# Performance work log

Measured on AMD Instinct MI355X. Metric: run time of the kernel, lower is better.

Reference implementation:

```python
import jax, jax.numpy as jnp
import numpy as np

D_MODEL = 1024
NUM_HEADS = 16
HEAD_DIM = D_MODEL // NUM_HEADS
ROPE_BASE = 10000.0


def setup_inputs() -> dict:
    key = jax.random.key(0)
    ks = jax.random.split(key, 9)
    B, S = 2, 2048
    x = jax.random.normal(ks[0], (B, S, D_MODEL), dtype=jnp.float32)
    s = 1.0 / np.sqrt(D_MODEL)
    Wq = jax.random.normal(ks[1], (D_MODEL, D_MODEL), dtype=jnp.float32) * s
    bq = jnp.zeros((D_MODEL,), dtype=jnp.float32)
    Wk = jax.random.normal(ks[2], (D_MODEL, D_MODEL), dtype=jnp.float32) * s
    bk = jnp.zeros((D_MODEL,), dtype=jnp.float32)
    Wv = jax.random.normal(ks[3], (D_MODEL, D_MODEL), dtype=jnp.float32) * s
    bv = jnp.zeros((D_MODEL,), dtype=jnp.float32)
    Wo = jax.random.normal(ks[4], (D_MODEL, D_MODEL), dtype=jnp.float32) * s
    bo = jnp.zeros((D_MODEL,), dtype=jnp.float32)
    return {"x": x, "Wq": Wq, "bq": bq, "Wk": Wk, "bk": bk,
            "Wv": Wv, "bv": bv, "Wo": Wo, "bo": bo}


def _apply_rope(x):
    # x: [B, H, S, Dh]; interleaved complex-pair RoPE (torch.view_as_complex style)
    B, H, S, Dh = x.shape
    inv_freq = 1.0 / (ROPE_BASE ** (jnp.arange(0, Dh, 2, dtype=jnp.float32) / Dh))
    pos = jnp.arange(S, dtype=jnp.float32)
    freqs = pos[:, None] * inv_freq[None, :]            # [S, Dh/2]
    cos, sin = jnp.cos(freqs), jnp.sin(freqs)           # each [S, Dh/2]
    x2 = x.reshape(B, H, S, Dh // 2, 2)
    xr, xi = x2[..., 0], x2[..., 1]
    out_r = xr * cos - xi * sin
    out_i = xr * sin + xi * cos
    return jnp.stack([out_r, out_i], axis=-1).reshape(B, H, S, Dh)


def reference(x, Wq, bq, Wk, bk, Wv, bv, Wo, bo):
    B, S, _ = x.shape
    H, Dh = NUM_HEADS, HEAD_DIM
    def proj(W, b):
        y = jnp.einsum('bsd,ed->bse', x, W) + b          # torch Linear: x @ W.T + b
        return y.reshape(B, S, H, Dh).transpose(0, 2, 1, 3)  # [B,H,S,Dh]
    Q = _apply_rope(proj(Wq, bq))
    K = _apply_rope(proj(Wk, bk))
    V = proj(Wv, bv)
    scale = 1.0 / jnp.sqrt(jnp.float32(Dh))
    scores = jnp.einsum('bhqd,bhkd->bhqk', Q, K) * scale
    causal = jnp.tril(jnp.ones((S, S), dtype=bool))
    scores = jnp.where(causal, scores, jnp.float32(-jnp.inf))
    attn = jax.nn.softmax(scores, axis=-1)
    out = jnp.einsum('bhqk,bhkd->bhqd', attn, V)         # [B,H,S,Dh]
    out = out.transpose(0, 2, 1, 3).reshape(B, S, H * Dh)
    return jnp.einsum('bsd,ed->bse', out, Wo) + bo
```

## Files before the change

### kernel.cpp

```cpp
#include <hip/hip_runtime.h>
#include <stdint.h>

#define S_LEN 2048
#define BATCH 2
#define DM 1024
#define NH 16
#define DH 64
#define MROWS 4096

typedef unsigned short u16;
typedef unsigned int u32;
typedef __attribute__((ext_vector_type(8))) short bf16x8;
typedef __attribute__((ext_vector_type(4))) float f32x4;
typedef __attribute__((ext_vector_type(2))) unsigned u32x2;

union pack8 { u32 w[4]; bf16x8 v8; };

__device__ inline u16 f2bf(float f) {
  union { float f; unsigned u; } v; v.f = f;
  unsigned u = v.u;
  unsigned r = u + 0x7fffu + ((u >> 16) & 1u);
  return (u16)(r >> 16);
}

__device__ inline u32 pkbf(float lo, float hi) {
  u32 r;
  asm("v_cvt_pk_bf16_f32 %0, %1, %2" : "=v"(r) : "v"(lo), "v"(hi));
  return r;
}

__device__ inline float bf2f(short s) {
  union { u32 u; float f; } c; c.u = ((u32)(u16)s) << 16;
  return c.f;
}

__device__ __forceinline__ void gload_lds16(const u16* g, u16* l) {
  __builtin_amdgcn_global_load_lds(
      (const __attribute__((address_space(1))) u32*)g,
      (__attribute__((address_space(3))) u32*)l, 16, 0, 0);
}

__global__ void convert_k(const float* __restrict__ x, const float* __restrict__ wq,
                          const float* __restrict__ wk, const float* __restrict__ wv,
                          const float* __restrict__ wo, u16* __restrict__ xb,
                          u16* __restrict__ wb) {
  int i = blockIdx.x * blockDim.x + threadIdx.x;
  const int total = (MROWS * DM + 4 * DM * DM) / 4;
  if (i >= total) return;
  int e = i * 4;
  const float* src;
  u16* dst;
  if (e < MROWS * DM) {
    src = x + e; dst = xb + e;
  } else {
    int j = e - MROWS * DM;
    int w = j >> 20;
    int o = j & ((1 << 20) - 1);
    src = (w == 0) ? wq + o : (w == 1) ? wk + o : (w == 2) ? wv + o : wo + o;
    dst = wb + j;
  }
  float4 v = *(const float4*)src;
  uint2 r;
  r.x = (unsigned)f2bf(v.x) | ((unsigned)f2bf(v.y) << 16);
  r.y = (unsigned)f2bf(v.z) | ((unsigned)f2bf(v.w) << 16);
  *(uint2*)dst = r;
}

__global__ void rope_k(float2* __restrict__ tab, float* __restrict__ kmax) {
  int i = blockIdx.x * blockDim.x + threadIdx.x;
  if (i < 32) kmax[i] = 0.f;
  if (i >= S_LEN * 32) return;
  int s = i >> 5, p = i & 31;
  float inv = expf(-(float)p * 0.28782313662425575f);
  float a = (float)s * inv;
  tab[i] = make_float2(cosf(a), sinf(a));
}

__global__ void knorm_k(const u16* __restrict__ K, float* __restrict__ kmax) {
  const int row = blockIdx.x * 256 + threadIdx.x;
  const int bh = row >> 11;
  const u16* p = K + (size_t)row * DH;
  float ss = 0.f;
#pragma unroll
  for (int i = 0; i < 8; i++) {
    bf16x8 v = *(const bf16x8*)(p + i * 8);
#pragma unroll
    for (int j = 0; j < 8; j++) { float f = bf2f(v[j]); ss += f * f; }
  }
  float kn = sqrtf(ss);
#pragma unroll
  for (int d = 1; d < 64; d <<= 1) kn = fmaxf(kn, __shfl_xor(kn, d));
  if ((threadIdx.x & 63) == 0)
    atomicMax((unsigned*)(kmax + bh), __float_as_uint(kn));
}

__launch_bounds__(256)
__global__ void gemm_k(const u16* __restrict__ A,
                       const u16* __restrict__ w0, const u16* __restrict__ w1,
                       const u16* __restrict__ w2,
                       const float* __restrict__ b0, const float* __restrict__ b1,
                       const float* __restrict__ b2,
                       const float2* __restrict__ rope,
                       void* __restrict__ o0, void* __restrict__ o1, void* __restrict__ o2,
                       int mode0) {
  const int mode = mode0 + (int)(blockIdx.x >> 8);
  const int tile = blockIdx.x & 255;
  const int mt = tile >> 3, nt = tile & 7;
  const int mbase = mt * 128, nbase = nt * 128;
  const u16* W = (mode == 1) ? w1 : (mode == 2) ? w2 : w0;
  const float* bias = (mode == 1) ? b1 : (mode == 2) ? b2 : b0;
  void* outp = (mode == 1) ? o1 : (mode == 2) ? o2 : o0;

  __shared__ u16 As[128 * 32];
  __shared__ u16 Bs[128 * 32];

  const int t = threadIdx.x;
  const int lane = t & 63, wvi = t >> 6;
  const int lr = lane & 15, lg = lane >> 4;
  const int wm = (wvi >> 1) * 64, wn = (wvi & 1) * 64;

  f32x4 acc[4][4] = {};
  const int srow = t >> 2;
  const int scol = (t & 3) * 8;

  for (int kk = 0; kk < DM; kk += 32) {
    gload_lds16(A + (size_t)(mbase + srow) * DM + kk + scol, &As[wvi * 512]);
    gload_lds16(A + (size_t)(mbase + 64 + srow) * DM + kk + scol, &As[2048 + wvi * 512]);
    gload_lds16(W + (size_t)(nbase + srow) * DM + kk + scol, &Bs[wvi * 512]);
    gload_lds16(W + (size_t)(nbase + 64 + srow) * DM + kk + scol, &Bs[2048 + wvi * 512]);
    __syncthreads();

    bf16x8 af[4], bfr[4];
#pragma unroll
    for (int mi = 0; mi < 4; mi++)
      af[mi] = *(const bf16x8*)&As[(wm + mi * 16 + lr) * 32 + lg * 8];
#pragma unroll
    for (int ni = 0; ni < 4; ni++)
      bfr[ni] = *(const bf16x8*)&Bs[(wn + ni * 16 + lr) * 32 + lg * 8];
#pragma unroll
    for (int mi = 0; mi < 4; mi++)
#pragma unroll
      for (int ni = 0; ni < 4; ni++)
        acc[mi][ni] = __builtin_amdgcn_mfma_f32_16x16x32_bf16(af[mi], bfr[ni], acc[mi][ni], 0, 0, 0);
    __syncthreads();
  }

#pragma unroll
  for (int ni = 0; ni < 4; ni++) {
    const int col = nbase + wn + ni * 16 + lr;
    const float bv = bias[col];
#pragma unroll
    for (int mi = 0; mi < 4; mi++) {
      const int row0 = mbase + wm + mi * 16 + lg * 4;
      f32x4 v = acc[mi][ni];
#pragma unroll
      for (int r = 0; r < 4; r++) {
        float val = v[r] + bv;
        const int row = row0 + r;
        if (mode <= 1) {
          float nb = __shfl_xor(val, 1);
          const int d = col & 63, p = d >> 1, s = row & (S_LEN - 1);
          float2 cs = rope[s * 32 + p];
          float ov = (d & 1) ? (nb * cs.y + val * cs.x) : (val * cs.x - nb * cs.y);
          if (mode == 0) ov *= 0.18033688011112042f;
          const int b = row >> 11, h = col >> 6;
          ((u16*)outp)[((size_t)(b * NH + h) * S_LEN + s) * DH + d] = f2bf(ov);
        } else if (mode == 2) {
          const int b = row >> 11, h = col >> 6, d = col & 63, s = row & (S_LEN - 1);
          const int j = s & 31;
          const int pos = (s & ~31) + (((j & 15) >> 2) << 3) + ((j >> 4) << 2) + (j & 3);
          ((u16*)outp)[((size_t)(b * NH + h) * DH + d) * S_LEN + pos] = f2bf(val);
        } else {
          ((float*)outp)[(size_t)row * DM + col] = val;
        }
      }
    }
  }
}

__device__ __forceinline__ void sm_pv(const float a[8], float m, float& l,
                                      bf16x8 v0, bf16x8 v1, bf16x8 v2, bf16x8 v3,
                                      f32x4* o) {
  float p[8];
#pragma unroll
  for (int r = 0; r < 8; r++) p[r] = __builtin_amdgcn_exp2f(a[r] - m);
  l += ((p[0] + p[1]) + (p[2] + p[3])) + ((p[4] + p[5]) + (p[6] + p[7]));
  pack8 pu;
  pu.w[0] = pkbf(p[0], p[1]);
  pu.w[1] = pkbf(p[2], p[3]);
  pu.w[2] = pkbf(p[4], p[5]);
  pu.w[3] = pkbf(p[6], p[7]);
  o[0] = __builtin_amdgcn_mfma_f32_16x16x32_bf16(v0, pu.v8, o[0], 0, 0, 0);
  o[1] = __builtin_amdgcn_mfma_f32_16x16x32_bf16(v1, pu.v8, o[1], 0, 0, 0);
  o[2] = __builtin_amdgcn_mfma_f32_16x16x32_bf16(v2, pu.v8, o[2], 0, 0, 0);
  o[3] = __builtin_amdgcn_mfma_f32_16x16x32_bf16(v3, pu.v8, o[3], 0, 0, 0);
}

__launch_bounds__(64)
__global__ void attn_k(const u16* __restrict__ Q, const u16* __restrict__ K,
                       const u16* __restrict__ Vt, u16* __restrict__ Oo,
                       const float* __restrict__ kmax,
                       u16* __restrict__ po, float* __restrict__ pl) {
  int bh, tile, s0, s1, pidx = 0, split;
  if (blockIdx.x < 1024) {
    bh = blockIdx.x & 31; tile = (int)(blockIdx.x >> 5);
    s0 = 0; s1 = tile + 1; split = 0;
  } else {
    const int idx = (int)blockIdx.x - 1024;
    bh = idx & 31; tile = 32 + ((idx >> 5) & 31);
    const int half = idx >> 10;
    const int nst = tile + 1, h = nst >> 1;
    s0 = half ? h : 0; s1 = half ? nst : h;
    pidx = idx; split = 1;
  }
  const int qbase = tile * 32;
  const int lane = threadIdx.x;
  const int lr = lane & 15, lg = lane >> 4;

  __shared__ u16 Ks[2][2048];
  __shared__ u16 Vs[2][2048];

  const u16* Kg = K + (size_t)bh * S_LEN * DH;
  const u16* Vg = Vt + (size_t)bh * DH * S_LEN;

  const int krow = lane >> 3;
  const int ksoff = ((((lane & 7) << 4) ^ ((lane >> 3) << 4)) >> 1);
  const int vrow = lane >> 2;
  const int vsoff = ((((lane & 3) << 4) ^ (((lane >> 3) & 3) << 4)) >> 1);

  const size_t qoff = ((size_t)bh * S_LEN + qbase + lr) * DH + lg * 8;
  const bf16x8 qA0 = *(const bf16x8*)(Q + qoff);
  const bf16x8 qA1 = *(const bf16x8*)(Q + qoff + 32);
  const bf16x8 qB0 = *(const bf16x8*)(Q + qoff + 16 * DH);
  const bf16x8 qB1 = *(const bf16x8*)(Q + qoff + 16 * DH + 32);

  float ssA = 0.f, ssB = 0.f;
#pragma unroll
  for (int j = 0; j < 8; j++) {
    float a0 = bf2f(qA0[j]), a1 = bf2f(qA1[j]);
    float b0 = bf2f(qB0[j]), b1 = bf2f(qB1[j]);
    ssA += a0 * a0 + a1 * a1;
    ssB += b0 * b0 + b1 * b1;
  }
  ssA += __shfl_xor(ssA, 16); ssA += __shfl_xor(ssA, 32);
  ssB += __shfl_xor(ssB, 16); ssB += __shfl_xor(ssB, 32);
  const float kmx = kmax[bh];
  const float mA = sqrtf(ssA) * kmx;
  const float mB = sqrtf(ssB) * kmx;

  f32x4 oA[4] = {}, oB[4] = {};
  float lA = 0.f, lB = 0.f;
  const f32x4 zero = {};

  const int kmsk = (lr & 7) << 4;
  const int k00 = lr * 64 + (((lg << 4)) ^ kmsk) / 2;
  const int k01 = lr * 64 + ((64 + (lg << 4)) ^ kmsk) / 2;
  const int k10 = (16 + lr) * 64 + (((lg << 4)) ^ kmsk) / 2;
  const int k11 = (16 + lr) * 64 + ((64 + (lg << 4)) ^ kmsk) / 2;
  const int vmsk = ((lr >> 1) & 3) << 4;
  const int vo = ((lg << 4) ^ vmsk) / 2;

#define STAGE(s32, bb)                                                          \
  {                                                                             \
    const u16* kgs = Kg + (size_t)(s32) * DH;                                   \
    const u16* vgs = Vg + (s32);                                                \
    _Pragma("unroll")                                                           \
    for (int i = 0; i < 4; i++)                                                 \
      gload_lds16(kgs + (size_t)(i * 8 + krow) * DH + ksoff, &Ks[bb][i * 512]); \
    _Pragma("unroll")                                                           \
    for (int i = 0; i < 4; i++)                                                 \
      gload_lds16(vgs + (size_t)(i * 16 + vrow) * S_LEN + vsoff, &Vs[bb][i * 512]); \
  }

  STAGE(s0 * 32, s0 & 1);

  for (int s = s0; s < s1; ++s) {
    const int b = s & 1;
    if (s + 1 < s1) {
      STAGE((s + 1) * 32, b ^ 1);
      asm volatile("s_waitcnt vmcnt(8)" ::: "memory");
    } else {
      asm volatile("s_waitcnt vmcnt(0)" ::: "memory");
    }

    const u16* Kb = Ks[b];
    const u16* Vb = Vs[b];
    bf16x8 kc0 = *(const bf16x8*)&Kb[k00];
    bf16x8 kc1 = *(const bf16x8*)&Kb[k01];
    bf16x8 kc2 = *(const bf16x8*)&Kb[k10];
    bf16x8 kc3 = *(const bf16x8*)&Kb[k11];
    bf16x8 v0 = *(const bf16x8*)&Vb[(lr) * 32 + vo];
    bf16x8 v1 = *(const bf16x8*)&Vb[(16 + lr) * 32 + vo];
    bf16x8 v2 = *(const bf16x8*)&Vb[(32 + lr) * 32 + vo];
    bf16x8 v3 = *(const bf16x8*)&Vb[(48 + lr) * 32 + vo];

    f32x4 s0A = __builtin_amdgcn_mfma_f32_16x16x32_bf16(kc0, qA0, zero, 0, 0, 0);
    s0A = __builtin_amdgcn_mfma_f32_16x16x32_bf16(kc1, qA1, s0A, 0, 0, 0);
    f32x4 s1A = __builtin_amdgcn_mfma_f32_16x16x32_bf16(kc2, qA0, zero, 0, 0, 0);
    s1A = __builtin_amdgcn_mfma_f32_16x16x32_bf16(kc3, qA1, s1A, 0, 0, 0);
    f32x4 s0B = __builtin_amdgcn_mfma_f32_16x16x32_bf16(kc0, qB0, zero, 0, 0, 0);
    s0B = __builtin_amdgcn_mfma_f32_16x16x32_bf16(kc1, qB1, s0B, 0, 0, 0);
    f32x4 s1B = __builtin_amdgcn_mfma_f32_16x16x32_bf16(kc2, qB0, zero, 0, 0, 0);
    s1B = __builtin_amdgcn_mfma_f32_16x16x32_bf16(kc3, qB1, s1B, 0, 0, 0);

    const int qrelA = qbase + lr - (s << 5) - (lg << 2);
    const int qrelB = qrelA + 16;
    float aA[8], aB[8];
#pragma unroll
    for (int r = 0; r < 4; r++) {
      aA[r]     = (r <= qrelA)      ? s0A[r] : -__builtin_inff();
      aA[4 + r] = (r + 16 <= qrelA) ? s1A[r] : -__builtin_inff();
      aB[r]     = (r <= qrelB)      ? s0B[r] : -__builtin_inff();
      aB[4 + r] = (r + 16 <= qrelB) ? s1B[r] : -__builtin_inff();
    }
    sm_pv(aA, mA, lA, v0, v1, v2, v3, oA);
    sm_pv(aB, mB, lB, v0, v1, v2, v3, oB);
  }
#undef STAGE

  lA += __shfl_xor(lA, 16); lA += __shfl_xor(lA, 32);
  lB += __shfl_xor(lB, 16); lB += __shfl_xor(lB, 32);

  if (!split) {
    const float rlA = __builtin_amdgcn_rcpf(lA);
    const float rlB = __builtin_amdgcn_rcpf(lB);
    const int bb = bh >> 4, h = bh & 15;
    const size_t obaseA = ((size_t)bb * S_LEN + qbase + lr) * DM + h * DH;
    const size_t obaseB = obaseA + (size_t)16 * DM;
#pragma unroll
    for (int dt = 0; dt < 4; dt++) {
      u32x2 pkA, pkB;
      pkA.x = pkbf(oA[dt][0] * rlA, oA[dt][1] * rlA);
      pkA.y = pkbf(oA[dt][2] * rlA, oA[dt][3] * rlA);
      pkB.x = pkbf(oB[dt][0] * rlB, oB[dt][1] * rlB);
      pkB.y = pkbf(oB[dt][2] * rlB, oB[dt][3] * rlB);
      *(u32x2*)(Oo + obaseA + dt * 16 + lg * 4) = pkA;
      *(u32x2*)(Oo + obaseB + dt * 16 + lg * 4) = pkB;
    }
  } else {
    u16* pb = po + (size_t)pidx * 2048;
#pragma unroll
    for (int dt = 0; dt < 4; dt++) {
      const int dbase = dt * 16 + lg * 4;
      u32x2 pkA, pkB;
      pkA.x = pkbf(oA[dt][0], oA[dt][1]);
      pkA.y = pkbf(oA[dt][2], oA[dt][3]);
      pkB.x = pkbf(oB[dt][0], oB[dt][1]);
      pkB.y = pkbf(oB[dt][2], oB[dt][3]);
      *(u32x2*)(pb + lr * 64 + dbase) = pkA;
      *(u32x2*)(pb + (16 + lr) * 64 + dbase) = pkB;
    }
    if (lg == 0) {
      pl[pidx * 32 + lr] = lA;
      pl[pidx * 32 + 16 + lr] = lB;
    }
  }
}

__global__ void reduce_k(const u16* __restrict__ po, const float* __restrict__ pl,
                         u16* __restrict__ Oo) {
  const int i = blockIdx.x * 256 + threadIdx.x;
  const int dg = i & 7;
  const int q = (i >> 3) & 31;
  const int tt = (i >> 8) & 31;
  const int bh = i >> 13;
  const int p0 = tt * 32 + bh, p1 = 1024 + p0;
  const bf16x8 a = *(const bf16x8*)(po + (size_t)p0 * 2048 + q * 64 + dg * 8);
  const bf16x8 b = *(const bf16x8*)(po + (size_t)p1 * 2048 + q * 64 + dg * 8);
  const float rl = __builtin_amdgcn_rcpf(pl[p0 * 32 + q] + pl[p1 * 32 + q]);
  pack8 r;
#pragma unroll
  for (int j = 0; j < 4; j++)
    r.w[j] = pkbf((bf2f(a[2 * j]) + bf2f(b[2 * j])) * rl,
                  (bf2f(a[2 * j + 1]) + bf2f(b[2 * j + 1])) * rl);
  const int s = (32 + tt) * 32 + q;
  u16* dst = Oo + ((size_t)(bh >> 4) * S_LEN + s) * DM + (bh & 15) * DH + dg * 8;
  *(bf16x8*)dst = r.v8;
}

extern "C" void kernel_launch(void* const* d_in, const int* in_sizes, int n_in,
                              void* d_out, int out_size, void* d_ws, size_t ws_size,
                              hipStream_t stream) {
  const float* x  = (const float*)d_in[0];
  const float* Wq = (const float*)d_in[1];
  const float* bq = (const float*)d_in[2];
  const float* Wk = (const float*)d_in[3];
  const float* bk = (const float*)d_in[4];
  const float* Wv = (const float*)d_in[5];
  const float* bv = (const float*)d_in[6];
  const float* Wo = (const float*)d_in[7];
  const float* bo = (const float*)d_in[8];

  char* ws = (char*)d_ws;
  u16* xb    = (u16*)(ws);
  u16* wb    = (u16*)(ws + (8u << 20));
  u16* Qb    = (u16*)(ws + (16u << 20));
  u16* Kb    = (u16*)(ws + (24u << 20));
  u16* Vtb   = (u16*)(ws + (32u << 20));
  u16* AOb   = (u16*)(ws + (40u << 20));
  float2* rt = (float2*)(ws + (48u << 20));
  float* kmx = (float*)(ws + (48u << 20) + (512u << 10));

  u16* po   = xb;
  float* pl = (float*)rt;

  convert_k<<<8192, 256, 0, stream>>>(x, Wq, Wk, Wv, Wo, xb, wb);
  rope_k<<<256, 256, 0, stream>>>(rt, kmx);
  gemm_k<<<768, 256, 0, stream>>>(xb, wb, wb + (1u << 20), wb + (2u << 20),
                                  bq, bk, bv, rt, Qb, Kb, Vtb, 0);
  knorm_k<<<256, 256, 0, stream>>>(Kb, kmx);
  attn_k<<<3072, 64, 0, stream>>>(Qb, Kb, Vtb, AOb, kmx, po, pl);
  reduce_k<<<1024, 256, 0, stream>>>(po, pl, AOb);
  gemm_k<<<256, 256, 0, stream>>>(AOb, wb + (3u << 20), wb + (3u << 20), wb + (3u << 20),
                                  bo, bo, bo, rt, d_out, d_out, d_out, 3);
}
```

Measured before the change: 149.7 us.

## Split output projection GEMM along K into two halves and add combine kernel

The output projection GEMM is split into two K-halves, which doubles its grid from 256 to 512 blocks so more CUs stay busy on MI355X. Each half writes bf16 partial sums into the reused Q/K buffers, and a new combine kernel adds the two partials plus the bias into the fp32 output. The tile index mapping is also remapped to a column-major order, which changes block scheduling for every GEMM. The cost is an extra kernel launch, extra memory traffic for the partials, and a loss of precision from rounding the partials to bf16.

Measured after the change: 154.7 us. +3.4%, slower.

```diff
diff --git a/kernel.cpp b/kernel.cpp
--- a/kernel.cpp
+++ b/kernel.cpp
@@ -103,8 +103,11 @@
                        const float2* __restrict__ rope,
                        void* __restrict__ o0, void* __restrict__ o1, void* __restrict__ o2,
                        int mode0) {
-  const int mode = mode0 + (int)(blockIdx.x >> 8);
-  const int tile = blockIdx.x & 255;
+  int mode, half = 0;
+  if (mode0 == 3) { mode = 3; half = (int)(blockIdx.x >> 8); }
+  else mode = mode0 + (int)(blockIdx.x >> 8);
+  const int t8 = blockIdx.x & 255;
+  const int tile = ((t8 & 7) << 5) | (t8 >> 3);
   const int mt = tile >> 3, nt = tile & 7;
   const int mbase = mt * 128, nbase = nt * 128;
   const u16* W = (mode == 1) ? w1 : (mode == 2) ? w2 : w0;
@@ -123,7 +126,10 @@
   const int srow = t >> 2;
   const int scol = (t & 3) * 8;
 
-  for (int kk = 0; kk < DM; kk += 32) {
+  const int kbeg = (mode == 3) ? (half << 9) : 0;
+  const int kend = kbeg + ((mode == 3) ? 512 : 1024);
+
+  for (int kk = kbeg; kk < kend; kk += 32) {
     gload_lds16(A + (size_t)(mbase + srow) * DM + kk + scol, &As[wvi * 512]);
     gload_lds16(A + (size_t)(mbase + 64 + srow) * DM + kk + scol, &As[2048 + wvi * 512]);
     gload_lds16(W + (size_t)(nbase + srow) * DM + kk + scol, &Bs[wvi * 512]);
@@ -148,7 +154,7 @@
 #pragma unroll
   for (int ni = 0; ni < 4; ni++) {
     const int col = nbase + wn + ni * 16 + lr;
-    const float bv = bias[col];
+    const float bv = (mode == 3) ? 0.f : bias[col];
 #pragma unroll
     for (int mi = 0; mi < 4; mi++) {
       const int row0 = mbase + wm + mi * 16 + lg * 4;
@@ -171,11 +177,34 @@
           const int pos = (s & ~31) + (((j & 15) >> 2) << 3) + ((j >> 4) << 2) + (j & 3);
           ((u16*)outp)[((size_t)(b * NH + h) * DH + d) * S_LEN + pos] = f2bf(val);
         } else {
-          ((float*)outp)[(size_t)row * DM + col] = val;
+          u16* pout = (u16*)(half ? o1 : o0);
+          pout[(size_t)row * DM + col] = f2bf(val);
         }
       }
     }
   }
+}
+
+__global__ void combine_k(const u16* __restrict__ p0, const u16* __restrict__ p1,
+                          const float* __restrict__ bo, float* __restrict__ out) {
+  const int i = blockIdx.x * 256 + threadIdx.x;
+  const int e = i * 8;
+  const bf16x8 a = *(const bf16x8*)(p0 + e);
+  const bf16x8 b = *(const bf16x8*)(p1 + e);
+  const int col = e & (DM - 1);
+  const float4 c0 = *(const float4*)(bo + col);
+  const float4 c1 = *(const float4*)(bo + col + 4);
+  float4 r0, r1;
+  r0.x = bf2f(a[0]) + bf2f(b[0]) + c0.x;
+  r0.y = bf2f(a[1]) + bf2f(b[1]) + c0.y;
+  r0.z = bf2f(a[2]) + bf2f(b[2]) + c0.z;
+  r0.w = bf2f(a[3]) + bf2f(b[3]) + c0.w;
+  r1.x = bf2f(a[4]) + bf2f(b[4]) + c1.x;
+  r1.y = bf2f(a[5]) + bf2f(b[5]) + c1.y;
+  r1.z = bf2f(a[6]) + bf2f(b[6]) + c1.z;
+  r1.w = bf2f(a[7]) + bf2f(b[7]) + c1.w;
+  *(float4*)(out + e) = r0;
+  *(float4*)(out + e + 4) = r1;
 }
 
 __device__ __forceinline__ void sm_pv(const float a[8], float m, float& l,
@@ -403,6 +432,8 @@
 
   u16* po   = xb;
   float* pl = (float*)rt;
+  u16* po30 = Qb;
+  u16* po31 = Kb;
 
   convert_k<<<8192, 256, 0, stream>>>(x, Wq, Wk, Wv, Wo, xb, wb);
   rope_k<<<256, 256, 0, stream>>>(rt, kmx);
@@ -411,6 +442,7 @@
   knorm_k<<<256, 256, 0, stream>>>(Kb, kmx);
   attn_k<<<3072, 64, 0, stream>>>(Qb, Kb, Vtb, AOb, kmx, po, pl);
   reduce_k<<<1024, 256, 0, stream>>>(po, pl, AOb);
-  gemm_k<<<256, 256, 0, stream>>>(AOb, wb + (3u << 20), wb + (3u << 20), wb + (3u << 20),
-                                  bo, bo, bo, rt, d_out, d_out, d_out, 3);
-}
+  gemm_k<<<512, 256, 0, stream>>>(AOb, wb + (3u << 20), wb + (3u << 20), wb + (3u << 20),
+                                  bo, bo, bo, rt, po30, po31, nullptr, 3);
+  combine_k<<<2048, 256, 0, stream>>>(po30, po31, bo, (float*)d_out);
+}
```
